# Optimization experiments

Measured on AMD Instinct MI355X. Metric: run time of the kernel, lower is better.

## Reference

```python
import jax, jax.numpy as jnp
import numpy as np

N = 50000; E = 1600000; W = 12; CIN = 32; CMID = 32; COUT = 32; K = 2; KER = 3; DIL = 1


def setup_inputs() -> dict:
    key = jax.random.key(0)
    ks = jax.random.split(key, 6)
    x = jax.random.normal(ks[0], (W, N, CIN), jnp.float32)
    A = jax.random.randint(ks[1], (2, E), 0, N, jnp.int32)
    Ew = jax.random.uniform(ks[2], (E,), jnp.float32)
    Wcheb = jax.random.normal(ks[3], (W, K, CIN, CMID), jnp.float32) / np.sqrt(CIN)
    bcheb = jnp.zeros((W, CMID), jnp.float32)
    Wconv = jax.random.normal(ks[4], (COUT, CMID, KER), jnp.float32) / np.sqrt(CMID * KER)
    bconv = jnp.zeros((COUT,), jnp.float32)
    return dict(x=x, A=A, Ew=Ew, Wcheb=Wcheb, bcheb=bcheb, Wconv=Wconv, bconv=bconv, batch_size=1)


def _prop(x, src, dst, w_hat):
    # one sparse matvec with L_hat per timestep; x: [W, N, C]
    msg = x[:, src, :] * w_hat[None, :, None]                      # [W, E, C]
    agg = jax.ops.segment_sum(msg.transpose(1, 0, 2), dst, num_segments=x.shape[1])  # [N, W, C]
    return agg.transpose(1, 0, 2)                                  # [W, N, C]


def reference(x, A, Ew, Wcheb, bcheb, Wconv, bconv, batch_size):
    src, dst = A[0], A[1]
    # sym-normalized Laplacian with lambda_max=2: L_hat = -D^{-1/2} A D^{-1/2}
    deg = jax.ops.segment_sum(Ew, dst, num_segments=x.shape[1])
    dinv = jnp.where(deg > 0, jax.lax.rsqrt(jnp.maximum(deg, 1e-12)), 0.0)
    w_hat = -dinv[src] * Ew * dinv[dst]

    # Chebyshev recurrence (vectorized over all window_size graphs at once)
    Txs = [x, _prop(x, src, dst, w_hat)]
    for _ in range(Wcheb.shape[1] - 2):
        Txs.append(2.0 * _prop(Txs[-1], src, dst, w_hat) - Txs[-2])

    out = bcheb[:, None, :]                                        # [W, 1, CMID]
    for k, Txk in enumerate(Txs):
        out = out + jnp.einsum('wnc,wcd->wnd', Txk, Wcheb[:, k])   # per-timestep weights

    # temporal Conv1d over the window axis: nodes act as conv batch
    h = out.transpose(1, 2, 0)                                     # [N, CMID, W]
    pad = (KER // 2) * DIL
    h = jax.lax.conv_general_dilated(h, Wconv, (1,), [(pad, pad)], rhs_dilation=(DIL,),
                                     dimension_numbers=('NCH', 'OIH', 'NCH'))
    h = h + bconv[None, :, None]
    h = h.transpose(0, 2, 1)                                       # [N, W, COUT]
    h = jnp.where(h >= 0, h, 0.01 * h)                             # LeakyReLU; dropout p=0 is identity
    return h
```

## Files before the change

kernel.cpp:

```cpp
#include <hip/hip_runtime.h>

#define WW 12
#define CH 32
#define KERN 3
#define ROWB 384
#define EBLK 2048

typedef __attribute__((ext_vector_type(8))) short short8v;
typedef __attribute__((ext_vector_type(4))) short short4v;
typedef __attribute__((ext_vector_type(4))) float f32x4;

__device__ __forceinline__ unsigned short bf16rne(float v) {
  unsigned int u = __float_as_uint(v);
  return (unsigned short)((u + 0x7FFFu + ((u >> 16) & 1u)) >> 16);
}
__device__ __forceinline__ float bf16tof(unsigned int b) {
  return __uint_as_float(b << 16);
}

__device__ __forceinline__ unsigned char fp8e4m3(float x) {
  unsigned int u = __float_as_uint(x);
  unsigned int s = (u >> 24) & 0x80u;
  float ax = fabsf(x);
  if (ax >= 464.f) return (unsigned char)(s | 0x7E);
  if (ax < 0.015625f) {
    int m = __float2int_rn(ax * 512.f);
    return (unsigned char)(s | (unsigned)m);
  }
  unsigned int au = u & 0x7fffffffu;
  au += 0x7FFFFu + ((au >> 20) & 1u);
  int e = (int)(au >> 23) - 127 + 7;
  unsigned int m = (au >> 20) & 7u;
  if (e > 15 || (e == 15 && m == 7)) return (unsigned char)(s | 0x7E);
  return (unsigned char)(s | ((unsigned)e << 3) | m);
}

__device__ __forceinline__ void dec4fma(unsigned int u, float wh, float* acc) {
#if __has_builtin(__builtin_amdgcn_cvt_pk_f32_fp8)
  auto lo = __builtin_amdgcn_cvt_pk_f32_fp8((int)u, false);
  auto hi = __builtin_amdgcn_cvt_pk_f32_fp8((int)u, true);
  acc[0] = fmaf(wh, lo[0], acc[0]);
  acc[1] = fmaf(wh, lo[1], acc[1]);
  acc[2] = fmaf(wh, hi[0], acc[2]);
  acc[3] = fmaf(wh, hi[1], acc[3]);
#else
#pragma unroll
  for (int j = 0; j < 4; ++j) {
    unsigned int b = (u >> (8 * j)) & 0xffu;
    float f = __uint_as_float(((b & 0x80u) << 24) | ((b & 0x7fu) << 20)) * 0x1.0p120f;
    acc[j] = fmaf(wh, f, acc[j]);
  }
#endif
}

__global__ __launch_bounds__(256) void histA_kernel(const int* __restrict__ dst,
                                                    int* __restrict__ blockhist,
                                                    int E, int NB) {
  __shared__ unsigned int hist[256];
  const int b = blockIdx.x;
  const int tid = threadIdx.x;
  hist[tid] = 0;
  __syncthreads();
  const int base = b * EBLK;
#pragma unroll
  for (int k = 0; k < EBLK / 256; ++k) {
    int e = base + k * 256 + tid;
    if (e < E) atomicAdd(&hist[(unsigned)dst[e] >> 8], 1u);
  }
  __syncthreads();
  blockhist[tid * NB + b] = (int)hist[tid];
}

__global__ void scanA_kernel(const int* __restrict__ in, int* __restrict__ bsum, int M) {
  __shared__ int red[256];
  int i = blockIdx.x * 256 + threadIdx.x;
  red[threadIdx.x] = (i < M) ? in[i] : 0;
  __syncthreads();
  for (int o = 128; o > 0; o >>= 1) {
    if (threadIdx.x < o) red[threadIdx.x] += red[threadIdx.x + o];
    __syncthreads();
  }
  if (threadIdx.x == 0) bsum[blockIdx.x] = red[0];
}
__global__ void scanB_kernel(int* __restrict__ bsum, int nb) {
  __shared__ int tmp[256];
  int tid = threadIdx.x;
  int chunk = (nb + 255) / 256;
  int lo = tid * chunk, hi = min(lo + chunk, nb);
  int s = 0;
  for (int i = lo; i < hi; ++i) s += bsum[i];
  tmp[tid] = s;
  __syncthreads();
  for (int o = 1; o < 256; o <<= 1) {
    int t = (tid >= o) ? tmp[tid - o] : 0;
    __syncthreads();
    tmp[tid] += t;
    __syncthreads();
  }
  int run = tmp[tid] - s;
  for (int i = lo; i < hi; ++i) {
    int v = bsum[i];
    bsum[i] = run;
    run += v;
  }
}
__global__ void scanC_kernel(const int* __restrict__ in, const int* __restrict__ bsum,
                             int* __restrict__ out, int M) {
  __shared__ int tmp[256];
  int tid = threadIdx.x;
  int i = blockIdx.x * 256 + tid;
  int v = (i < M) ? in[i] : 0;
  tmp[tid] = v;
  __syncthreads();
  for (int o = 1; o < 256; o <<= 1) {
    int t = (tid >= o) ? tmp[tid - o] : 0;
    __syncthreads();
    tmp[tid] += t;
    __syncthreads();
  }
  if (i < M) out[i] = bsum[blockIdx.x] + tmp[tid] - v;
}

__global__ __launch_bounds__(256) void scatpack_kernel(
    const int* __restrict__ src, const int* __restrict__ dst, const float* __restrict__ Ew,
    const int* __restrict__ scanout, unsigned long long* __restrict__ rec8,
    const float* __restrict__ x, const float* __restrict__ Wcheb,
    const float* __restrict__ Wconv,
    unsigned short* __restrict__ xt, unsigned char* __restrict__ xq,
    unsigned short* __restrict__ wb01, unsigned short* __restrict__ wbc,
    int E, int N, int NB, int npackTot, int npx) {
  if ((int)blockIdx.x < NB) {
    const int b = blockIdx.x;
    __shared__ int pos[256];
    const int tid = threadIdx.x;
    pos[tid] = scanout[tid * NB + b];
    __syncthreads();
    int e = b * EBLK + tid;
    bool valid = e < E;
    int d = 0, s = 0;
    float w = 0.f;
    if (valid) { d = dst[e]; s = src[e]; w = Ew[e]; }
#pragma unroll
    for (int k = 0; k < EBLK / 256; ++k) {
      int e2 = e + 256;
      bool v2 = (k + 1 < EBLK / 256) && (e2 < E);
      int d2 = 0, s2 = 0;
      float w2 = 0.f;
      if (v2) { d2 = dst[e2]; s2 = src[e2]; w2 = Ew[e2]; }
      if (valid) {
        int bucket = (unsigned)d >> 8;
        int p = atomicAdd(&pos[bucket], 1);
        rec8[p] = ((unsigned long long)(unsigned)d << 32) |
                  ((unsigned)s << 16) | bf16rne(w);
      }
      e = e2; d = d2; s = s2; w = w2; valid = v2;
    }
    return;
  }
  int pid = blockIdx.x - NB;
  if (pid >= npackTot) return;
  if (pid < npx) {
    long long f = ((long long)pid * 256 + threadIdx.x) * 8;
    const long long T = (long long)WW * N * CH;
    if (f >= T) return;
    float4 v0 = *(const float4*)(x + f);
    float4 v1 = *(const float4*)(x + f + 4);
    int w = (int)(f / ((long long)N * CH));
    int rem = (int)(f - (long long)w * N * CH);
    int n = rem >> 5;
    int c = rem & 31;
    size_t o = (size_t)n * ROWB + w * CH + c;
    short4v h0, h1;
    h0[0] = (short)bf16rne(v0.x); h0[1] = (short)bf16rne(v0.y);
    h0[2] = (short)bf16rne(v0.z); h0[3] = (short)bf16rne(v0.w);
    h1[0] = (short)bf16rne(v1.x); h1[1] = (short)bf16rne(v1.y);
    h1[2] = (short)bf16rne(v1.z); h1[3] = (short)bf16rne(v1.w);
    *(short4v*)(xt + o) = h0;
    *(short4v*)(xt + o + 4) = h1;
    unsigned int q0 = (unsigned int)fp8e4m3(v0.x) | ((unsigned int)fp8e4m3(v0.y) << 8) |
                      ((unsigned int)fp8e4m3(v0.z) << 16) | ((unsigned int)fp8e4m3(v0.w) << 24);
    unsigned int q1 = (unsigned int)fp8e4m3(v1.x) | ((unsigned int)fp8e4m3(v1.y) << 8) |
                      ((unsigned int)fp8e4m3(v1.z) << 16) | ((unsigned int)fp8e4m3(v1.w) << 24);
    *(unsigned int*)(xq + o) = q0;
    *(unsigned int*)(xq + o + 4) = q1;
    return;
  }
  int id = (pid - npx) * 256 + threadIdx.x;
  if (id < 12 * 2 * 2 * 64 * 8) {
    int j = id & 7, l = (id >> 3) & 63, h = (id >> 9) & 1, m = (id >> 10) & 1, ww = id >> 11;
    int k = ((l >> 4) << 3) + j;
    int d = (l & 15) + (h << 4);
    wb01[id] = bf16rne(Wcheb[((size_t)(ww * 2 + m) * 32 + k) * 32 + d]);
  } else if (id < 24576 + 3 * 2 * 64 * 8) {
    int i2 = id - 24576;
    int j = i2 & 7, l = (i2 >> 3) & 63, h = (i2 >> 9) & 1, k = i2 >> 10;
    int c = ((l >> 4) << 3) + j;
    int o = (l & 15) + (h << 4);
    wbc[i2] = bf16rne(Wconv[((size_t)(o * 32 + c)) * 3 + k]);
  }
}

__global__ __launch_bounds__(256) void passB_kernel(
    const unsigned long long* __restrict__ rec8, const int* __restrict__ scanout,
    int* __restrict__ rowptr, float* __restrict__ dinv,
    unsigned int* __restrict__ epair, int N, int E, int NB) {
  __shared__ unsigned int hist[256];
  __shared__ unsigned int qsum[256];
  __shared__ int sub[256];
  __shared__ int tmp[256];
  const int B = blockIdx.x;
  const int tid = threadIdx.x;
  hist[tid] = 0;
  qsum[tid] = 0;
  __syncthreads();
  const int bstart = scanout[B * NB];
  const int bend = scanout[(B + 1) * NB];
  {
    int i = bstart + tid;
    unsigned long long r = (i < bend) ? rec8[i] : 0;
    while (i < bend) {
      int i2 = i + 256;
      unsigned long long r2 = (i2 < bend) ? rec8[i2] : 0;
      int low = (int)((r >> 32) & 255u);
      atomicAdd(&hist[low], 1u);
      unsigned int q = (unsigned int)__float2int_rn(bf16tof((unsigned int)r & 0xffffu) * 16777216.f);
      atomicAdd(&qsum[low], q);
      i = i2; r = r2;
    }
  }
  __syncthreads();
  int v = (int)hist[tid];
  tmp[tid] = v;
  __syncthreads();
  for (int o = 1; o < 256; o <<= 1) {
    int t = (tid >= o) ? tmp[tid - o] : 0;
    __syncthreads();
    tmp[tid] += t;
    __syncthreads();
  }
  sub[tid] = tmp[tid] - v;
  int n = (B << 8) + tid;
  if (n < N) {
    rowptr[n] = bstart + sub[tid];
    float deg = (float)qsum[tid] * (1.f / 16777216.f);
    dinv[n] = (deg > 0.f) ? rsqrtf(fmaxf(deg, 1e-12f)) : 0.f;
  }
  if (B == 0 && tid == 0) rowptr[N] = E;
  __syncthreads();
  tmp[tid] = bstart + sub[tid];
  __syncthreads();
  {
    int i = bstart + tid;
    unsigned long long r = (i < bend) ? rec8[i] : 0;
    while (i < bend) {
      int i2 = i + 256;
      unsigned long long r2 = (i2 < bend) ? rec8[i2] : 0;
      int low = (int)((r >> 32) & 255u);
      int p = atomicAdd(&tmp[low], 1);
      epair[p] = (unsigned int)r;
      i = i2; r = r2;
    }
  }
}

__global__ __launch_bounds__(256) void gather_kernel(
    const int* __restrict__ rowptr, const unsigned int* __restrict__ epair,
    const float* __restrict__ dinv,
    const unsigned char* __restrict__ xq, unsigned short* __restrict__ zt, int N) {
  int gt = blockIdx.x * blockDim.x + threadIdx.x;
  int n = gt >> 6;
  if (n >= N) return;
  int lane = gt & 63;
  int half = lane >> 5;
  int l = lane & 31;

  const float ndinv = -dinv[n];

  float acc[WW];
#pragma unroll
  for (int j = 0; j < WW; ++j) acc[j] = 0.f;

  int i = rowptr[n] + half;
  const int i1 = rowptr[n + 1];
  for (; i + 6 < i1; i += 8) {
    unsigned int e0 = epair[i];
    unsigned int e1 = epair[i + 2];
    unsigned int e2 = epair[i + 4];
    unsigned int e3 = epair[i + 6];
    const unsigned int* p0 = (const unsigned int*)(xq + (size_t)(e0 >> 16) * ROWB + l * 12);
    const unsigned int* p1 = (const unsigned int*)(xq + (size_t)(e1 >> 16) * ROWB + l * 12);
    const unsigned int* p2 = (const unsigned int*)(xq + (size_t)(e2 >> 16) * ROWB + l * 12);
    const unsigned int* p3 = (const unsigned int*)(xq + (size_t)(e3 >> 16) * ROWB + l * 12);
    unsigned int a0 = p0[0], a1 = p0[1], a2 = p0[2];
    unsigned int b0 = p1[0], b1 = p1[1], b2 = p1[2];
    unsigned int c0 = p2[0], c1 = p2[1], c2 = p2[2];
    unsigned int d0 = p3[0], d1 = p3[1], d2 = p3[2];
    float w0 = ndinv * bf16tof(e0 & 0xffffu) * dinv[e0 >> 16];
    float w1 = ndinv * bf16tof(e1 & 0xffffu) * dinv[e1 >> 16];
    float w2 = ndinv * bf16tof(e2 & 0xffffu) * dinv[e2 >> 16];
    float w3 = ndinv * bf16tof(e3 & 0xffffu) * dinv[e3 >> 16];
    dec4fma(a0, w0, acc + 0); dec4fma(a1, w0, acc + 4); dec4fma(a2, w0, acc + 8);
    dec4fma(b0, w1, acc + 0); dec4fma(b1, w1, acc + 4); dec4fma(b2, w1, acc + 8);
    dec4fma(c0, w2, acc + 0); dec4fma(c1, w2, acc + 4); dec4fma(c2, w2, acc + 8);
    dec4fma(d0, w3, acc + 0); dec4fma(d1, w3, acc + 4); dec4fma(d2, w3, acc + 8);
  }
  for (; i < i1; i += 2) {
    unsigned int e0 = epair[i];
    const unsigned int* p0 = (const unsigned int*)(xq + (size_t)(e0 >> 16) * ROWB + l * 12);
    unsigned int a0 = p0[0], a1 = p0[1], a2 = p0[2];
    float w0 = ndinv * bf16tof(e0 & 0xffffu) * dinv[e0 >> 16];
    dec4fma(a0, w0, acc + 0); dec4fma(a1, w0, acc + 4); dec4fma(a2, w0, acc + 8);
  }
#pragma unroll
  for (int j = 0; j < WW; ++j) acc[j] += __shfl_xor(acc[j], 32);

  if (half == 0) {
    unsigned short* q = zt + (size_t)n * ROWB + l * 12;
    short4v o0, o1, o2;
#pragma unroll
    for (int j = 0; j < 4; ++j) {
      o0[j] = (short)bf16rne(acc[j]);
      o1[j] = (short)bf16rne(acc[4 + j]);
      o2[j] = (short)bf16rne(acc[8 + j]);
    }
    *(short4v*)(q) = o0;
    *(short4v*)(q + 4) = o1;
    *(short4v*)(q + 8) = o2;
  }
}

__global__ __launch_bounds__(256) void mc_kernel(
    const unsigned short* __restrict__ xt, const unsigned short* __restrict__ zt,
    const unsigned short* __restrict__ wb01, const unsigned short* __restrict__ wbc,
    const float* __restrict__ bcheb, const float* __restrict__ bconv,
    float* __restrict__ out, int N) {
  __shared__ __align__(16) unsigned short hts[4][4][16][40];
  const int wid = threadIdx.x >> 6;
  const int lane = threadIdx.x & 63;
  const int n0 = (blockIdx.x * 4 + wid) * 16;
  if (n0 >= N) return;
  const int kg = lane >> 4;
  const int arow = lane & 15;
  const int rrow = min(n0 + arow, N - 1);

  short8v wcf0[3], wcf1[3];
#pragma unroll
  for (int k = 0; k < 3; ++k) {
    wcf0[k] = *(const short8v*)(wbc + (((k * 2 + 0) * 64 + lane) << 3));
    wcf1[k] = *(const short8v*)(wbc + (((k * 2 + 1) * 64 + lane) << 3));
  }
  const float bc0 = bconv[arow];
  const float bc1 = bconv[arow + 16];

  auto computeH = [&](int w) {
    const size_t fofs = (size_t)rrow * ROWB + w * CH + kg * 8;
    short8v xf = *(const short8v*)(xt + fofs);
    short8v zf = *(const short8v*)(zt + fofs);
    unsigned short* hrow = &hts[wid][w & 3][0][0];
#pragma unroll
    for (int h = 0; h < 2; ++h) {
      short8v w0f = *(const short8v*)(wb01 + ((((w * 2 + 0) * 2 + h) * 64 + lane) << 3));
      short8v w1f = *(const short8v*)(wb01 + ((((w * 2 + 1) * 2 + h) * 64 + lane) << 3));
      f32x4 acc = {0.f, 0.f, 0.f, 0.f};
      acc = __builtin_amdgcn_mfma_f32_16x16x32_bf16(xf, w0f, acc, 0, 0, 0);
      acc = __builtin_amdgcn_mfma_f32_16x16x32_bf16(zf, w1f, acc, 0, 0, 0);
      const int d = arow + (h << 4);
      const float bias = bcheb[w * CH + d];
#pragma unroll
      for (int r = 0; r < 4; ++r) {
        hrow[(kg * 4 + r) * 40 + d] = bf16rne(acc[r] + bias);
      }
    }
  };

  auto convT = [&](int t) {
    f32x4 a0 = {0.f, 0.f, 0.f, 0.f};
    f32x4 a1 = {0.f, 0.f, 0.f, 0.f};
#pragma unroll
    for (int k = 0; k < 3; ++k) {
      int w = t + k - 1;
      if (w < 0 || w >= WW) continue;
      short8v hf = *(const short8v*)(&hts[wid][w & 3][arow][kg * 8]);
      a0 = __builtin_amdgcn_mfma_f32_16x16x32_bf16(hf, wcf0[k], a0, 0, 0, 0);
      a1 = __builtin_amdgcn_mfma_f32_16x16x32_bf16(hf, wcf1[k], a1, 0, 0, 0);
    }
#pragma unroll
    for (int r = 0; r < 4; ++r) {
      int node = n0 + kg * 4 + r;
      if (node >= N) continue;
      float v0 = a0[r] + bc0;
      float v1 = a1[r] + bc1;
      v0 = (v0 >= 0.f) ? v0 : 0.01f * v0;
      v1 = (v1 >= 0.f) ? v1 : 0.01f * v1;
      size_t o = ((size_t)node * WW + t) * CH;
      out[o + arow] = v0;
      out[o + arow + 16] = v1;
    }
  };

  computeH(0);
  computeH(1);
  convT(0);
  for (int w = 2; w < WW; ++w) {
    computeH(w);
    convT(w - 1);
  }
  convT(WW - 1);
}

extern "C" void kernel_launch(void* const* d_in, const int* in_sizes, int n_in,
                              void* d_out, int out_size, void* d_ws, size_t ws_size,
                              hipStream_t stream) {
  const float* x     = (const float*)d_in[0];
  const int*   A     = (const int*)d_in[1];
  const float* Ew    = (const float*)d_in[2];
  const float* Wcheb = (const float*)d_in[3];
  const float* bcheb = (const float*)d_in[4];
  const float* Wconv = (const float*)d_in[5];
  const float* bconv = (const float*)d_in[6];
  float* out = (float*)d_out;

  const int E = in_sizes[2];
  const int N = in_sizes[0] / (WW * CH);
  const int* srcA = A;
  const int* dstA = A + E;

  char* ws = (char*)d_ws;
  size_t off = 0;
  auto alloc = [&](size_t bytes) -> void* {
    void* p = ws + off;
    off += (bytes + 255) / 256 * 256;
    return p;
  };
  const int NB = (E + EBLK - 1) / EBLK;
  const int M = 256 * NB;
  const int NBUCK = (N + 255) / 256;

  int* blockhist = (int*)alloc((size_t)M * 4);
  int* scanout   = (int*)alloc((size_t)(M + 1) * 4);
  int* bsum      = (int*)alloc((size_t)((M + 255) / 256) * 4);
  int* rowptr    = (int*)alloc((size_t)(N + 1) * 4);
  float* dinv    = (float*)alloc((size_t)N * 4);
  unsigned long long* rec8 = (unsigned long long*)alloc((size_t)E * 8);
  unsigned int* epair = (unsigned int*)alloc((size_t)E * 4);
  unsigned short* xt   = (unsigned short*)alloc((size_t)N * ROWB * 2);
  unsigned char*  xq   = (unsigned char*)alloc((size_t)N * ROWB);
  unsigned short* zt   = (unsigned short*)alloc((size_t)N * ROWB * 2);
  unsigned short* wb01 = (unsigned short*)alloc((size_t)24576 * 2);
  unsigned short* wbc  = (unsigned short*)alloc((size_t)3072 * 2);
  (void)ws_size;

  histA_kernel<<<NB, 256, 0, stream>>>(dstA, blockhist, E, NB);

  const int nbs = (M + 255) / 256;
  scanA_kernel<<<nbs, 256, 0, stream>>>(blockhist, bsum, M);
  scanB_kernel<<<1, 256, 0, stream>>>(bsum, nbs);
  scanC_kernel<<<nbs, 256, 0, stream>>>(blockhist, bsum, scanout, M);

  const long long T = (long long)WW * N * CH;
  const int npx = (int)((T + 2047) / 2048);
  const int nwb = (24576 + 3072 + 255) / 256;
  const int npackTot = npx + nwb;
  scatpack_kernel<<<NB + npackTot, 256, 0, stream>>>(
      srcA, dstA, Ew, scanout, rec8, x, Wcheb, Wconv, xt, xq, wb01, wbc,
      E, N, NB, npackTot, npx);

  passB_kernel<<<NBUCK, 256, 0, stream>>>(rec8, scanout, rowptr, dinv, epair, N, E, NB);

  long long gtot = (long long)N * 64;
  gather_kernel<<<(unsigned)((gtot + 255) / 256), 256, 0, stream>>>(rowptr, epair, dinv, xq, zt, N);

  int ntiles = (N + 15) / 16;
  int mcblocks = (ntiles + 3) / 4;
  mc_kernel<<<mcblocks, 256, 0, stream>>>(xt, zt, wb01, wbc, bcheb, bconv, out, N);
}
```

Before: 209.3 us.

## Fold source dinv into fp8 features and apply destination dinv after gather

Degree is now accumulated with global atomics in the histogram kernel, and dinv is computed in a small new kernel before packing. The fp8 copy of x is pre-scaled by dinv[src], and the gather applies -dinv[dst] once per output row. This removes the per-edge random dinv load and multiply from the gather inner loop, which is also unrolled deeper (8 edges per half-wave). In exchange it adds 1.6M global atomics, an extra memset and kernel launch, and quantises dinv-scaled values to fp8, which changes rounding.

Result: slower. 278.8 us (+33.2%).

```diff
diff --git a/kernel.cpp b/kernel.cpp
--- a/kernel.cpp
+++ b/kernel.cpp
@@ -54,6 +54,8 @@
 }
 
 __global__ __launch_bounds__(256) void histA_kernel(const int* __restrict__ dst,
+                                                    const float* __restrict__ Ew,
+                                                    unsigned int* __restrict__ degq,
                                                     int* __restrict__ blockhist,
                                                     int E, int NB) {
   __shared__ unsigned int hist[256];
@@ -65,10 +67,23 @@
 #pragma unroll
   for (int k = 0; k < EBLK / 256; ++k) {
     int e = base + k * 256 + tid;
-    if (e < E) atomicAdd(&hist[(unsigned)dst[e] >> 8], 1u);
+    if (e < E) {
+      int d = dst[e];
+      atomicAdd(&hist[(unsigned)d >> 8], 1u);
+      atomicAdd(&degq[d], (unsigned int)__float2int_rn(Ew[e] * 16777216.f));
+    }
   }
   __syncthreads();
   blockhist[tid * NB + b] = (int)hist[tid];
+}
+
+__global__ void dinv_kernel(const unsigned int* __restrict__ degq,
+                            float* __restrict__ dinv, int N) {
+  int n = blockIdx.x * blockDim.x + threadIdx.x;
+  if (n < N) {
+    float deg = (float)degq[n] * (1.f / 16777216.f);
+    dinv[n] = (deg > 0.f) ? rsqrtf(fmaxf(deg, 1e-12f)) : 0.f;
+  }
 }
 
 __global__ void scanA_kernel(const int* __restrict__ in, int* __restrict__ bsum, int M) {
@@ -124,8 +139,8 @@
 __global__ __launch_bounds__(256) void scatpack_kernel(
     const int* __restrict__ src, const int* __restrict__ dst, const float* __restrict__ Ew,
     const int* __restrict__ scanout, unsigned long long* __restrict__ rec8,
-    const float* __restrict__ x, const float* __restrict__ Wcheb,
-    const float* __restrict__ Wconv,
+    const float* __restrict__ x, const float* __restrict__ dinv,
+    const float* __restrict__ Wcheb, const float* __restrict__ Wconv,
     unsigned short* __restrict__ xt, unsigned char* __restrict__ xq,
     unsigned short* __restrict__ wb01, unsigned short* __restrict__ wbc,
     int E, int N, int NB, int npackTot, int npx) {
@@ -169,6 +184,7 @@
     int rem = (int)(f - (long long)w * N * CH);
     int n = rem >> 5;
     int c = rem & 31;
+    const float dn = dinv[n];
     size_t o = (size_t)n * ROWB + w * CH + c;
     short4v h0, h1;
     h0[0] = (short)bf16rne(v0.x); h0[1] = (short)bf16rne(v0.y);
@@ -177,10 +193,10 @@
     h1[2] = (short)bf16rne(v1.z); h1[3] = (short)bf16rne(v1.w);
     *(short4v*)(xt + o) = h0;
     *(short4v*)(xt + o + 4) = h1;
-    unsigned int q0 = (unsigned int)fp8e4m3(v0.x) | ((unsigned int)fp8e4m3(v0.y) << 8) |
-                      ((unsigned int)fp8e4m3(v0.z) << 16) | ((unsigned int)fp8e4m3(v0.w) << 24);
-    unsigned int q1 = (unsigned int)fp8e4m3(v1.x) | ((unsigned int)fp8e4m3(v1.y) << 8) |
-                      ((unsigned int)fp8e4m3(v1.z) << 16) | ((unsigned int)fp8e4m3(v1.w) << 24);
+    unsigned int q0 = (unsigned int)fp8e4m3(v0.x * dn) | ((unsigned int)fp8e4m3(v0.y * dn) << 8) |
+                      ((unsigned int)fp8e4m3(v0.z * dn) << 16) | ((unsigned int)fp8e4m3(v0.w * dn) << 24);
+    unsigned int q1 = (unsigned int)fp8e4m3(v1.x * dn) | ((unsigned int)fp8e4m3(v1.y * dn) << 8) |
+                      ((unsigned int)fp8e4m3(v1.z * dn) << 16) | ((unsigned int)fp8e4m3(v1.w * dn) << 24);
     *(unsigned int*)(xq + o) = q0;
     *(unsigned int*)(xq + o + 4) = q1;
     return;
@@ -202,16 +218,13 @@
 
 __global__ __launch_bounds__(256) void passB_kernel(
     const unsigned long long* __restrict__ rec8, const int* __restrict__ scanout,
-    int* __restrict__ rowptr, float* __restrict__ dinv,
-    unsigned int* __restrict__ epair, int N, int E, int NB) {
+    int* __restrict__ rowptr, unsigned int* __restrict__ epair, int N, int E, int NB) {
   __shared__ unsigned int hist[256];
-  __shared__ unsigned int qsum[256];
   __shared__ int sub[256];
   __shared__ int tmp[256];
   const int B = blockIdx.x;
   const int tid = threadIdx.x;
   hist[tid] = 0;
-  qsum[tid] = 0;
   __syncthreads();
   const int bstart = scanout[B * NB];
   const int bend = scanout[(B + 1) * NB];
@@ -221,10 +234,7 @@
     while (i < bend) {
       int i2 = i + 256;
       unsigned long long r2 = (i2 < bend) ? rec8[i2] : 0;
-      int low = (int)((r >> 32) & 255u);
-      atomicAdd(&hist[low], 1u);
-      unsigned int q = (unsigned int)__float2int_rn(bf16tof((unsigned int)r & 0xffffu) * 16777216.f);
-      atomicAdd(&qsum[low], q);
+      atomicAdd(&hist[(int)((r >> 32) & 255u)], 1u);
       i = i2; r = r2;
     }
   }
@@ -240,11 +250,7 @@
   }
   sub[tid] = tmp[tid] - v;
   int n = (B << 8) + tid;
-  if (n < N) {
-    rowptr[n] = bstart + sub[tid];
-    float deg = (float)qsum[tid] * (1.f / 16777216.f);
-    dinv[n] = (deg > 0.f) ? rsqrtf(fmaxf(deg, 1e-12f)) : 0.f;
-  }
+  if (n < N) rowptr[n] = bstart + sub[tid];
   if (B == 0 && tid == 0) rowptr[N] = E;
   __syncthreads();
   tmp[tid] = bstart + sub[tid];
@@ -274,54 +280,67 @@
   int half = lane >> 5;
   int l = lane & 31;
 
-  const float ndinv = -dinv[n];
-
   float acc[WW];
 #pragma unroll
   for (int j = 0; j < WW; ++j) acc[j] = 0.f;
 
   int i = rowptr[n] + half;
   const int i1 = rowptr[n + 1];
+  for (; i + 14 < i1; i += 16) {
+    unsigned int er[8];
+#pragma unroll
+    for (int u = 0; u < 8; ++u) er[u] = epair[i + 2 * u];
+    unsigned int dw[8][3];
+#pragma unroll
+    for (int u = 0; u < 8; ++u) {
+      const unsigned int* p = (const unsigned int*)(xq + (size_t)(er[u] >> 16) * ROWB + l * 12);
+      dw[u][0] = p[0]; dw[u][1] = p[1]; dw[u][2] = p[2];
+    }
+#pragma unroll
+    for (int u = 0; u < 8; ++u) {
+      float w = bf16tof(er[u] & 0xffffu);
+      dec4fma(dw[u][0], w, acc + 0);
+      dec4fma(dw[u][1], w, acc + 4);
+      dec4fma(dw[u][2], w, acc + 8);
+    }
+  }
   for (; i + 6 < i1; i += 8) {
-    unsigned int e0 = epair[i];
-    unsigned int e1 = epair[i + 2];
-    unsigned int e2 = epair[i + 4];
-    unsigned int e3 = epair[i + 6];
-    const unsigned int* p0 = (const unsigned int*)(xq + (size_t)(e0 >> 16) * ROWB + l * 12);
-    const unsigned int* p1 = (const unsigned int*)(xq + (size_t)(e1 >> 16) * ROWB + l * 12);
-    const unsigned int* p2 = (const unsigned int*)(xq + (size_t)(e2 >> 16) * ROWB + l * 12);
-    const unsigned int* p3 = (const unsigned int*)(xq + (size_t)(e3 >> 16) * ROWB + l * 12);
-    unsigned int a0 = p0[0], a1 = p0[1], a2 = p0[2];
-    unsigned int b0 = p1[0], b1 = p1[1], b2 = p1[2];
-    unsigned int c0 = p2[0], c1 = p2[1], c2 = p2[2];
-    unsigned int d0 = p3[0], d1 = p3[1], d2 = p3[2];
-    float w0 = ndinv * bf16tof(e0 & 0xffffu) * dinv[e0 >> 16];
-    float w1 = ndinv * bf16tof(e1 & 0xffffu) * dinv[e1 >> 16];
-    float w2 = ndinv * bf16tof(e2 & 0xffffu) * dinv[e2 >> 16];
-    float w3 = ndinv * bf16tof(e3 & 0xffffu) * dinv[e3 >> 16];
-    dec4fma(a0, w0, acc + 0); dec4fma(a1, w0, acc + 4); dec4fma(a2, w0, acc + 8);
-    dec4fma(b0, w1, acc + 0); dec4fma(b1, w1, acc + 4); dec4fma(b2, w1, acc + 8);
-    dec4fma(c0, w2, acc + 0); dec4fma(c1, w2, acc + 4); dec4fma(c2, w2, acc + 8);
-    dec4fma(d0, w3, acc + 0); dec4fma(d1, w3, acc + 4); dec4fma(d2, w3, acc + 8);
+    unsigned int er[4];
+#pragma unroll
+    for (int u = 0; u < 4; ++u) er[u] = epair[i + 2 * u];
+    unsigned int dw[4][3];
+#pragma unroll
+    for (int u = 0; u < 4; ++u) {
+      const unsigned int* p = (const unsigned int*)(xq + (size_t)(er[u] >> 16) * ROWB + l * 12);
+      dw[u][0] = p[0]; dw[u][1] = p[1]; dw[u][2] = p[2];
+    }
+#pragma unroll
+    for (int u = 0; u < 4; ++u) {
+      float w = bf16tof(er[u] & 0xffffu);
+      dec4fma(dw[u][0], w, acc + 0);
+      dec4fma(dw[u][1], w, acc + 4);
+      dec4fma(dw[u][2], w, acc + 8);
+    }
   }
   for (; i < i1; i += 2) {
     unsigned int e0 = epair[i];
     const unsigned int* p0 = (const unsigned int*)(xq + (size_t)(e0 >> 16) * ROWB + l * 12);
     unsigned int a0 = p0[0], a1 = p0[1], a2 = p0[2];
-    float w0 = ndinv * bf16tof(e0 & 0xffffu) * dinv[e0 >> 16];
+    float w0 = bf16tof(e0 & 0xffffu);
     dec4fma(a0, w0, acc + 0); dec4fma(a1, w0, acc + 4); dec4fma(a2, w0, acc + 8);
   }
 #pragma unroll
   for (int j = 0; j < WW; ++j) acc[j] += __shfl_xor(acc[j], 32);
 
   if (half == 0) {
+    const float ndinv = -dinv[n];
     unsigned short* q = zt + (size_t)n * ROWB + l * 12;
     short4v o0, o1, o2;
 #pragma unroll
     for (int j = 0; j < 4; ++j) {
-      o0[j] = (short)bf16rne(acc[j]);
-      o1[j] = (short)bf16rne(acc[4 + j]);
-      o2[j] = (short)bf16rne(acc[8 + j]);
+      o0[j] = (short)bf16rne(acc[j] * ndinv);
+      o1[j] = (short)bf16rne(acc[4 + j] * ndinv);
+      o2[j] = (short)bf16rne(acc[8 + j] * ndinv);
     }
     *(short4v*)(q) = o0;
     *(short4v*)(q + 4) = o1;
@@ -436,11 +455,12 @@
   const int M = 256 * NB;
   const int NBUCK = (N + 255) / 256;
 
+  unsigned int* degq = (unsigned int*)alloc((size_t)N * 4);
+  float* dinv    = (float*)alloc((size_t)N * 4);
   int* blockhist = (int*)alloc((size_t)M * 4);
   int* scanout   = (int*)alloc((size_t)(M + 1) * 4);
   int* bsum      = (int*)alloc((size_t)((M + 255) / 256) * 4);
   int* rowptr    = (int*)alloc((size_t)(N + 1) * 4);
-  float* dinv    = (float*)alloc((size_t)N * 4);
   unsigned long long* rec8 = (unsigned long long*)alloc((size_t)E * 8);
   unsigned int* epair = (unsigned int*)alloc((size_t)E * 4);
   unsigned short* xt   = (unsigned short*)alloc((size_t)N * ROWB * 2);
@@ -450,7 +470,10 @@
   unsigned short* wbc  = (unsigned short*)alloc((size_t)3072 * 2);
   (void)ws_size;
 
-  histA_kernel<<<NB, 256, 0, stream>>>(dstA, blockhist, E, NB);
+  hipMemsetAsync(degq, 0, (size_t)N * 4, stream);
+
+  histA_kernel<<<NB, 256, 0, stream>>>(dstA, Ew, degq, blockhist, E, NB);
+  dinv_kernel<<<(N + 255) / 256, 256, 0, stream>>>(degq, dinv, N);
 
   const int nbs = (M + 255) / 256;
   scanA_kernel<<<nbs, 256, 0, stream>>>(blockhist, bsum, M);
@@ -462,10 +485,10 @@
   const int nwb = (24576 + 3072 + 255) / 256;
   const int npackTot = npx + nwb;
   scatpack_kernel<<<NB + npackTot, 256, 0, stream>>>(
-      srcA, dstA, Ew, scanout, rec8, x, Wcheb, Wconv, xt, xq, wb01, wbc,
+      srcA, dstA, Ew, scanout, rec8, x, dinv, Wcheb, Wconv, xt, xq, wb01, wbc,
       E, N, NB, npackTot, npx);
 
-  passB_kernel<<<NBUCK, 256, 0, stream>>>(rec8, scanout, rowptr, dinv, epair, N, E, NB);
+  passB_kernel<<<NBUCK, 256, 0, stream>>>(rec8, scanout, rowptr, epair, N, E, NB);
 
   long long gtot = (long long)N * 64;
   gather_kernel<<<(unsigned)((gtot + 255) / 256), 256, 0, stream>>>(rowptr, epair, dinv, xq, zt, N);
```
